# Performance work log

Hardware: AMD Instinct MI355X
Metric: run time of the kernel (lower is better)

The kernel has to match this reference:

```python
import jax, jax.numpy as jnp
import numpy as np

B, F, H, C, K = 4096, 1536, 256, 38, 7  # nodes, feat_dim(effnet_b3), hidden, classes, knn k
EPS = 1e-5  # BatchNorm eps


def setup_inputs() -> dict:
    key = jax.random.key(0)
    ks = jax.random.split(key, 20)
    r = lambda i, shape, s=1.0: jax.random.normal(ks[i], shape, jnp.float32) * s
    u = lambda i, shape: jax.random.uniform(ks[i], shape, jnp.float32, 0.5, 1.5)
    inp = {
        "features": r(0, (B, F)),          # CNN backbone output
        "noise": r(1, (B, B)),             # tie-break noise (scaled by 1e-6 inside)
        # BatchNorm1d on CNN features (eval mode: running stats)
        "bnf_g": jnp.ones((F,)), "bnf_b": jnp.zeros((F,)),
        "bnf_m": r(2, (F,), 0.1), "bnf_v": u(3, (F,)),
        # GCNConv weights
        "W1": r(4, (F, H), 0.02), "b1": jnp.zeros((H,)),
        "W2": r(5, (H, H), 0.05), "b2": jnp.zeros((H,)),
        "W3": r(6, (H, H), 0.05), "b3": jnp.zeros((H,)),
        # PyG BatchNorms (eval mode)
        "bn1_g": jnp.ones((H,)), "bn1_b": jnp.zeros((H,)), "bn1_m": r(7, (H,), 0.1), "bn1_v": u(8, (H,)),
        "bn2_g": jnp.ones((H,)), "bn2_b": jnp.zeros((H,)), "bn2_m": r(9, (H,), 0.1), "bn2_v": u(10, (H,)),
        "bn3_g": jnp.ones((H,)), "bn3_b": jnp.zeros((H,)), "bn3_m": r(11, (H,), 0.1), "bn3_v": u(12, (H,)),
        # classifier MLP
        "Wc1": r(13, (H + F, H // 2), 0.02), "bc1": jnp.zeros((H // 2,)),
        "Wc2": r(14, (H // 2, C), 0.05), "bc2": jnp.zeros((C,)),
    }
    return inp


def _bn(x, g, b, m, v):
    return (x - m) * jax.lax.rsqrt(v + EPS) * g + b


def _knn_edges(x, noise):
    # torch.cdist (p=2) + 1e-6 noise + topk smallest; drop self (col 0)
    sq = jnp.sum(x * x, axis=1)
    d2 = jnp.maximum(sq[:, None] + sq[None, :] - 2.0 * (x @ x.T), 0.0)
    d = jnp.sqrt(d2) + noise * 1e-6
    _, idx = jax.lax.top_k(-d, K + 1)          # smallest K+1 distances
    knn = idx[:, 1:]                           # [B, K] neighbors (col 0 = self)
    src = jnp.repeat(jnp.arange(B), K)         # edge i -> j as in edge_list [[i, j]]
    dst = knn.reshape(-1)
    return src, dst


def _gcn(x, src, dst, W, b):
    # GCNConv: add self-loops, symmetric normalization, aggregate at target (dst)
    h = x @ W
    loop = jnp.arange(B)
    s = jnp.concatenate([src, loop])
    t = jnp.concatenate([dst, loop])
    deg = jnp.zeros((B,), x.dtype).at[t].add(1.0)
    dinv = jax.lax.rsqrt(deg)                  # deg >= 1 due to self-loops
    norm = dinv[s] * dinv[t]
    out = jnp.zeros_like(h).at[t].add(norm[:, None] * h[s])
    return out + b


def reference(features, noise, bnf_g, bnf_b, bnf_m, bnf_v,
              W1, b1, W2, b2, W3, b3,
              bn1_g, bn1_b, bn1_m, bn1_v,
              bn2_g, bn2_b, bn2_m, bn2_v,
              bn3_g, bn3_b, bn3_m, bn3_v,
              Wc1, bc1, Wc2, bc2):
    # CNN head: BN (eval) + dropout(identity in eval)
    x = _bn(features, bnf_g, bnf_b, bnf_m, bnf_v)
    src, dst = _knn_edges(jax.lax.stop_gradient(x), noise)
    x_orig = x
    h = jax.nn.relu(_bn(_gcn(x, src, dst, W1, b1), bn1_g, bn1_b, bn1_m, bn1_v))
    h = jax.nn.relu(_bn(_gcn(h, src, dst, W2, b2), bn2_g, bn2_b, bn2_m, bn2_v))
    h = _bn(_gcn(h, src, dst, W3, b3), bn3_g, bn3_b, bn3_m, bn3_v)
    # batch = arange(B) => global_mean_pool is identity per node
    comb = jnp.concatenate([h, x_orig], axis=1)        # [B, H+F]
    hid = jax.nn.relu(comb @ Wc1 + bc1)
    return hid @ Wc2 + bc2                             # [B, num_classes]
```

## Files before the change

kernel.cpp:

```cpp
#include <hip/hip_runtime.h>
#include <hip/hip_bf16.h>
#include <math.h>

#define Bn 4096
#define Fn 1536
#define Hn 256
#define Cn 38
#define Kn 7
#define GBK 64
#define NCAND 12

typedef __attribute__((ext_vector_type(8))) short short8;
typedef __attribute__((ext_vector_type(4))) float f32x4;
typedef unsigned long long u64;
typedef unsigned int u32;
typedef unsigned short u16;

__device__ __forceinline__ void gld16(const void* g, void* l) {
  __builtin_amdgcn_global_load_lds((const __attribute__((address_space(1))) unsigned int*)g,
                                   (__attribute__((address_space(3))) unsigned int*)l, 16, 0, 0);
}

__global__ void k_prep(const float* __restrict__ g, const float* __restrict__ b,
                       const float* __restrict__ m, const float* __restrict__ v,
                       double* __restrict__ A64, double* __restrict__ C64) {
  int f = blockIdx.x * 256 + threadIdx.x;
  if (f < Fn) {
    double rs = 1.0 / sqrt((double)v[f] + 1e-5);
    double a = (double)g[f] * rs;
    A64[f] = a;
    C64[f] = (double)b[f] - (double)m[f] * a;
  }
}

__global__ void k_bnsplit(const float* __restrict__ feat, const double* __restrict__ A64,
                          const double* __restrict__ C64,
                          u16* __restrict__ Ah, u16* __restrict__ Al, double* __restrict__ sq,
                          float* __restrict__ deg) {
  int row = blockIdx.x;
  int f0 = threadIdx.x * 8;
  const float* fr = feat + (size_t)row * Fn + f0;
  float4 a = *reinterpret_cast<const float4*>(fr);
  float4 b = *reinterpret_cast<const float4*>(fr + 4);
  float xs[8] = {a.x, a.y, a.z, a.w, b.x, b.y, b.z, b.w};
  short8 hv, lv;
  double ss = 0.0;
#pragma unroll
  for (int k = 0; k < 8; k++) {
    double xd = fma((double)xs[k], A64[f0 + k], C64[f0 + k]);
    ss = fma(xd, xd, ss);
    float x = (float)xd;
    __hip_bfloat16 h = __float2bfloat16(x);
    float hf = __bfloat162float(h);
    __hip_bfloat16 lo = __float2bfloat16(x - hf);
    hv[k] = (short)*reinterpret_cast<u16*>(&h);
    lv[k] = (short)*reinterpret_cast<u16*>(&lo);
  }
  *reinterpret_cast<short8*>(Ah + (size_t)row * Fn + f0) = hv;
  *reinterpret_cast<short8*>(Al + (size_t)row * Fn + f0) = lv;
#pragma unroll
  for (int o = 32; o; o >>= 1) ss += __shfl_down(ss, o);
  __shared__ double red[3];
  if ((threadIdx.x & 63) == 0) red[threadIdx.x >> 6] = ss;
  __syncthreads();
  if (threadIdx.x == 0) { sq[row] = red[0] + red[1] + red[2]; deg[row] = 1.f; }
}

__global__ void k_wsplit_all(
    const float* __restrict__ W1, const float* __restrict__ W2, const float* __restrict__ W3,
    const float* __restrict__ Wc1, const float* __restrict__ Wc2,
    u16* __restrict__ W1th, u16* __restrict__ W1tl, u16* __restrict__ W2th, u16* __restrict__ W2tl,
    u16* __restrict__ W3th, u16* __restrict__ W3tl, u16* __restrict__ Wc1th, u16* __restrict__ Wc1tl,
    u16* __restrict__ Wc2th, u16* __restrict__ Wc2tl) {
  const float* W; u16 *Th, *Tl; int K, N;
  switch (blockIdx.z) {
    case 0: W = W1;  Th = W1th;  Tl = W1tl;  K = Fn;      N = Hn;  break;
    case 1: W = W2;  Th = W2th;  Tl = W2tl;  K = Hn;      N = Hn;  break;
    case 2: W = W3;  Th = W3th;  Tl = W3tl;  K = Hn;      N = Hn;  break;
    case 3: W = Wc1; Th = Wc1th; Tl = Wc1tl; K = Hn + Fn; N = 128; break;
    default: W = Wc2; Th = Wc2th; Tl = Wc2tl; K = 128;    N = Cn;  break;
  }
  int k0 = blockIdx.y * 32, n0 = blockIdx.x * 32;
  if (k0 >= K || n0 >= N) return;
  __shared__ float t[32][33];
  int tx = threadIdx.x & 31, ty = threadIdx.x >> 5;
  for (int p = 0; p < 32; p += 8) {
    int k = k0 + ty + p, n = n0 + tx;
    t[ty + p][tx] = (k < K && n < N) ? W[(size_t)k * N + n] : 0.f;
  }
  __syncthreads();
  for (int p = 0; p < 32; p += 8) {
    int n = n0 + ty + p, k = k0 + tx;
    if (n < N && k < K) {
      float x = t[tx][ty + p];
      __hip_bfloat16 h = __float2bfloat16(x);
      float hf = __bfloat162float(h);
      __hip_bfloat16 lo = __float2bfloat16(x - hf);
      Th[(size_t)n * K + k] = *reinterpret_cast<u16*>(&h);
      Tl[(size_t)n * K + k] = *reinterpret_cast<u16*>(&lo);
    }
  }
}

__global__ __launch_bounds__(256) void k_gram(
    const u16* __restrict__ Ah, const double* __restrict__ sq, u64* __restrict__ part) {
  __shared__ union {
    u16 t[2][4096];
    float c[64 * 65];
  } lds;
  const int tid = threadIdx.x;
  const int w = tid >> 6, l = tid & 63;

  int xcd = blockIdx.x & 7;
  int s = blockIdx.x >> 3;
  int ti, tj;
  if (s < 36) {
    int rem = s, a_ = 0;
#pragma unroll 1
    while (rem >= 8 - a_) { rem -= 8 - a_; a_++; }
    ti = xcd * 8 + a_;
    tj = xcd * 8 + a_ + rem;
  } else {
    int sp = s - 36;
    int q = sp >> 6, r = sp & 63;
    int op, l64;
    if (q < 3) { op = xcd * 3 + q; l64 = r; }
    else       { op = 24 + (xcd >> 1); l64 = ((xcd & 1) << 5) | r; }
    int rem = op, g = 0;
#pragma unroll 1
    while (rem >= 7 - g) { rem -= 7 - g; g++; }
    int gi = g, gj = g + 1 + rem;
    ti = gi * 8 + (l64 >> 3);
    tj = gj * 8 + (l64 & 7);
  }
  const int rA0 = ti * 64, rB0 = tj * 64;
  const int isDiag = (ti == tj);

  f32x4 acc[2][2];
  const f32x4 fz = {0.f, 0.f, 0.f, 0.f};
#pragma unroll
  for (int i = 0; i < 2; i++)
#pragma unroll
    for (int j = 0; j < 2; j++) acc[i][j] = fz;

  const u16* mats[2] = { Ah + (size_t)rA0 * Fn, Ah + (size_t)rB0 * Fn };

  auto stage = [&](int k0) {
#pragma unroll
    for (int q = 0; q < 4; q++) {
      int idx = w * 4 + q;
      int mm = idx >> 3, kh = (idx >> 2) & 1, sg = idx & 3;
      int row = sg * 16 + (l >> 2);
      int colel = ((l & 3) * 8) ^ (((l >> 3) & 3) * 8);
      gld16(mats[mm] + (size_t)row * Fn + k0 + kh * 32 + colel,
            (char*)&lds.t[mm][0] + kh * 4096 + sg * 1024);
    }
  };

  const int cB = ((l >> 4) * 16) ^ (((l >> 1) & 3) * 16);
  const int fr16 = l & 15;

  stage(0);
  const int NT = Fn / GBK;
  for (int kt = 0; kt < NT; kt++) {
    __syncthreads();
#pragma unroll
    for (int kh = 0; kh < 2; kh++) {
      short8 fa[2], fb[2];
#pragma unroll
      for (int i = 0; i < 2; i++) {
        int ar = (w >> 1) * 32 + i * 16 + fr16;
        fa[i] = *reinterpret_cast<const short8*>((const char*)&lds.t[0][0] + kh * 4096 + ar * 64 + cB);
        int br = (w & 1) * 32 + i * 16 + fr16;
        fb[i] = *reinterpret_cast<const short8*>((const char*)&lds.t[1][0] + kh * 4096 + br * 64 + cB);
      }
#pragma unroll
      for (int i = 0; i < 2; i++)
#pragma unroll
        for (int j = 0; j < 2; j++)
          acc[i][j] = __builtin_amdgcn_mfma_f32_16x16x32_bf16(fa[i], fb[j], acc[i][j], 0, 0, 0);
    }
    __syncthreads();
    if (kt + 1 < NT) stage((kt + 1) * GBK);
  }

  const int fr = l & 15, fq = l >> 4;
#pragma unroll
  for (int i = 0; i < 2; i++) {
    int r0 = (w >> 1) * 32 + i * 16 + fq * 4;
#pragma unroll
    for (int j = 0; j < 2; j++) {
      int c0 = (w & 1) * 32 + j * 16 + fr;
#pragma unroll
      for (int gg = 0; gg < 4; gg++)
        lds.c[(r0 + gg) * 65 + c0] = acc[i][j][gg];
    }
  }
  __syncthreads();

  u64 top[8];
#pragma unroll
  for (int k = 0; k < 8; k++) top[k] = ~0ull;
  if (tid < 64) {
    int grow = rA0 + tid;
    float sqr = (float)sq[grow];
#pragma unroll 1
    for (int c = 0; c < 64; c++) {
      int gc = rB0 + c;
      if (gc == grow) continue;
      float gv = lds.c[tid * 65 + c];
      float d2 = fmaxf(sqr + (float)sq[gc] - 2.f * gv, 0.f);
      u64 key = ((u64)__float_as_uint(d2) << 32) | (u32)gc;
      if (key < top[7]) {
        top[7] = key;
#pragma unroll
        for (int k = 7; k > 0; k--)
          if (top[k] < top[k - 1]) { u64 tmp = top[k]; top[k] = top[k - 1]; top[k - 1] = tmp; }
      }
    }
    u64* dst = part + ((size_t)grow * 64 + tj) * 8;
#pragma unroll
    for (int k = 0; k < 8; k++) dst[k] = top[k];
  } else if (tid < 128 && !isDiag) {
    int cl = tid - 64;
    int gcol = rB0 + cl;
    float sqc = (float)sq[gcol];
#pragma unroll 1
    for (int s2 = 0; s2 < 64; s2++) {
      float gv = lds.c[s2 * 65 + cl];
      int gr = rA0 + s2;
      float d2 = fmaxf(sqc + (float)sq[gr] - 2.f * gv, 0.f);
      u64 key = ((u64)__float_as_uint(d2) << 32) | (u32)gr;
      if (key < top[7]) {
        top[7] = key;
#pragma unroll
        for (int k = 7; k > 0; k--)
          if (top[k] < top[k - 1]) { u64 tmp = top[k]; top[k] = top[k - 1]; top[k - 1] = tmp; }
      }
    }
    u64* dst = part + ((size_t)gcol * 64 + ti) * 8;
#pragma unroll
    for (int k = 0; k < 8; k++) dst[k] = top[k];
  }
}

__global__ __launch_bounds__(256) void k_candmerge(const u64* __restrict__ part,
                                                   int* __restrict__ cand) {
  int row = blockIdx.x * 4 + (threadIdx.x >> 6);
  int l = threadIdx.x & 63;
  const u64* p = part + (size_t)row * 512 + (size_t)l * 8;
  u64 e[8];
#pragma unroll
  for (int k = 0; k < 8; k++) e[k] = p[k];
#pragma unroll 1
  for (int rnd = 0; rnd < NCAND; rnd++) {
    u64 m = e[0];
#pragma unroll
    for (int k = 1; k < 8; k++) m = e[k] < m ? e[k] : m;
#pragma unroll
    for (int off = 32; off; off >>= 1) {
      u64 o = __shfl_xor(m, off);
      m = o < m ? o : m;
    }
    if (l == 0) cand[row * NCAND + rnd] = (int)(u32)m;
#pragma unroll
    for (int k = 0; k < 8; k++)
      if (e[k] == m) e[k] = ~0ull;
  }
}

__global__ __launch_bounds__(256) void k_rerank(
    const float* __restrict__ feat, const double* __restrict__ A64,
    const double* __restrict__ C64, const double* __restrict__ sq,
    const float* __restrict__ noise, const int* __restrict__ cand,
    int* __restrict__ knn, float* __restrict__ deg) {
  int row = blockIdx.x;
  int w = threadIdx.x >> 6, l = threadIdx.x & 63;
  double xr[Fn / 64];
  const float* fr = feat + (size_t)row * Fn;
#pragma unroll
  for (int i = 0; i < Fn / 64; i++) {
    int e = l + 64 * i;
    xr[i] = fma((double)fr[e], A64[e], C64[e]);
  }
  __shared__ double dots[NCAND];
  for (int m = w; m < NCAND; m += 4) {
    int c = cand[row * NCAND + m];
    const float* fc = feat + (size_t)c * Fn;
    double s = 0.0;
#pragma unroll
    for (int i = 0; i < Fn / 64; i++) {
      int e = l + 64 * i;
      double xj = fma((double)fc[e], A64[e], C64[e]);
      s = fma(xr[i], xj, s);
    }
#pragma unroll
    for (int off = 32; off; off >>= 1) s += __shfl_xor(s, off);
    if (l == 0) dots[m] = s;
  }
  __syncthreads();
  if (threadIdx.x == 0) {
    double sr = sq[row];
    double bd[Kn]; int bi7[Kn];
#pragma unroll
    for (int k = 0; k < Kn; k++) { bd[k] = 1e300; bi7[k] = 0; }
#pragma unroll 1
    for (int m = 0; m < NCAND; m++) {
      int c = cand[row * NCAND + m];
      double d2 = sr + sq[c] - 2.0 * dots[m];
      d2 = d2 > 0.0 ? d2 : 0.0;
      double d = sqrt(d2) + (double)noise[(size_t)row * Bn + c] * 1e-6;
      if (d < bd[Kn - 1]) {
        bd[Kn - 1] = d; bi7[Kn - 1] = c;
#pragma unroll
        for (int k = Kn - 1; k > 0; k--)
          if (bd[k] < bd[k - 1]) {
            double td = bd[k]; bd[k] = bd[k - 1]; bd[k - 1] = td;
            int ti = bi7[k]; bi7[k] = bi7[k - 1]; bi7[k - 1] = ti;
          }
      }
    }
#pragma unroll
    for (int k = 0; k < Kn; k++) {
      knn[row * Kn + k] = bi7[k];
      atomicAdd(&deg[bi7[k]], 1.f);
    }
  }
}

__global__ void k_dinv(const float* __restrict__ deg, float* __restrict__ dinv) {
  int i = blockIdx.x * 256 + threadIdx.x;
  if (i < Bn) dinv[i] = rsqrtf(deg[i]);
}

__global__ void k_aggsc(const float* __restrict__ h, const int* __restrict__ knn,
                        const float* __restrict__ dinv, float* __restrict__ out) {
  int s = blockIdx.x, f = threadIdx.x;
  float hv = h[(size_t)s * Hn + f] * dinv[s];
#pragma unroll
  for (int k = 0; k < Kn; k++) {
    int t = knn[s * Kn + k];
    atomicAdd(&out[(size_t)t * Hn + f], dinv[t] * hv);
  }
}

__global__ void k_bnact_split(const float* __restrict__ x, const float* __restrict__ g,
                              const float* __restrict__ b, const float* __restrict__ m,
                              const float* __restrict__ v, int relu,
                              u16* __restrict__ oh, u16* __restrict__ ol) {
  size_t i8 = ((size_t)blockIdx.x * 256 + threadIdx.x) * 8;
  int c0 = (int)(i8 & (Hn - 1));
  float4 a = *reinterpret_cast<const float4*>(x + i8);
  float4 bb = *reinterpret_cast<const float4*>(x + i8 + 4);
  float xs[8] = {a.x, a.y, a.z, a.w, bb.x, bb.y, bb.z, bb.w};
  short8 hv, lv;
#pragma unroll
  for (int k = 0; k < 8; k++) {
    int c = c0 + k;
    float val = (xs[k] - m[c]) * rsqrtf(v[c] + 1e-5f) * g[c] + b[c];
    if (relu) val = fmaxf(val, 0.f);
    __hip_bfloat16 h = __float2bfloat16(val);
    float hf = __bfloat162float(h);
    __hip_bfloat16 lo = __float2bfloat16(val - hf);
    hv[k] = (short)*reinterpret_cast<u16*>(&h);
    lv[k] = (short)*reinterpret_cast<u16*>(&lo);
  }
  *reinterpret_cast<short8*>(oh + i8) = hv;
  *reinterpret_cast<short8*>(ol + i8) = lv;
}

__global__ __launch_bounds__(256) void k_mgemm(
    const u16* __restrict__ Ah1, const u16* __restrict__ Al1, int lda1,
    const u16* __restrict__ Ah2, const u16* __restrict__ Al2, int lda2, int Ksplit,
    const u16* __restrict__ Wth, const u16* __restrict__ Wtl,
    const float* __restrict__ bias, float* __restrict__ C, int N, int K, int ep,
    float* __restrict__ C2, const float* __restrict__ dinvp,
    u16* __restrict__ OH, u16* __restrict__ OL) {
  __shared__ u16 tA[2][2][4096];
  __shared__ u16 tB[2][2][4096];
  const int tid = threadIdx.x;
  const int w = tid >> 6, l = tid & 63;
  const int m0 = blockIdx.y * 64, n0 = blockIdx.x * 64;
  const int fr = l & 15, fq = l >> 4;

  f32x4 acc[2][2];
  const f32x4 fz = {0.f, 0.f, 0.f, 0.f};
#pragma unroll
  for (int i = 0; i < 2; i++)
#pragma unroll
    for (int j = 0; j < 2; j++) acc[i][j] = fz;

  auto stage = [&](int buf, int k0) {
#pragma unroll
    for (int q = 0; q < 2; q++) {
      int s = w * 2 + q;
      int kg = k0 + s * 8;
      const u16* ah; const u16* al; int ld; int kk = kg;
      if (kg < Ksplit) { ah = Ah1; al = Al1; ld = lda1; }
      else             { ah = Ah2; al = Al2; ld = lda2; kk = kg - Ksplit; }
      gld16(ah + (size_t)(m0 + l) * ld + kk, (char*)&tA[buf][0][0] + s * 1024);
      gld16(al + (size_t)(m0 + l) * ld + kk, (char*)&tA[buf][1][0] + s * 1024);
      gld16(Wth + (size_t)(n0 + l) * K + kg, (char*)&tB[buf][0][0] + s * 1024);
      gld16(Wtl + (size_t)(n0 + l) * K + kg, (char*)&tB[buf][1][0] + s * 1024);
    }
  };

  stage(0, 0);
  const int NT = K / GBK;
  int cur = 0;
  for (int kt = 0; kt < NT; kt++) {
    __syncthreads();
    if (kt + 1 < NT) stage(cur ^ 1, (kt + 1) * GBK);
#pragma unroll
    for (int kh = 0; kh < 2; kh++) {
      const int kb = (kh * 4 + fq) * 1024;
      short8 fa[2][2], fb[2][2];
#pragma unroll
      for (int i = 0; i < 2; i++) {
        int ar = (w >> 1) * 32 + i * 16 + fr;
        fa[0][i] = *reinterpret_cast<const short8*>((const char*)&tA[cur][0][0] + kb + ar * 16);
        fa[1][i] = *reinterpret_cast<const short8*>((const char*)&tA[cur][1][0] + kb + ar * 16);
        int br = (w & 1) * 32 + i * 16 + fr;
        fb[0][i] = *reinterpret_cast<const short8*>((const char*)&tB[cur][0][0] + kb + br * 16);
        fb[1][i] = *reinterpret_cast<const short8*>((const char*)&tB[cur][1][0] + kb + br * 16);
      }
#pragma unroll
      for (int i = 0; i < 2; i++)
#pragma unroll
        for (int j = 0; j < 2; j++) {
          acc[i][j] = __builtin_amdgcn_mfma_f32_16x16x32_bf16(fa[1][i], fb[0][j], acc[i][j], 0, 0, 0);
          acc[i][j] = __builtin_amdgcn_mfma_f32_16x16x32_bf16(fa[0][i], fb[1][j], acc[i][j], 0, 0, 0);
          acc[i][j] = __builtin_amdgcn_mfma_f32_16x16x32_bf16(fa[0][i], fb[0][j], acc[i][j], 0, 0, 0);
        }
    }
    cur ^= 1;
  }

#pragma unroll
  for (int i = 0; i < 2; i++) {
    int rg0 = m0 + (w >> 1) * 32 + i * 16 + fq * 4;
#pragma unroll
    for (int j = 0; j < 2; j++) {
      int cg = n0 + (w & 1) * 32 + j * 16 + fr;
      if (cg >= N) continue;
      float bv = (ep >= 1) ? bias[cg] : 0.f;
#pragma unroll
      for (int g = 0; g < 4; g++) {
        float raw = acc[i][j][g];
        size_t idx = (size_t)(rg0 + g) * N + cg;
        if (ep == 3) {
          float di = dinvp[rg0 + g];
          C[idx] = raw;
          C2[idx] = di * di * raw + bv;
        } else if (ep == 4) {
          float val = fmaxf(raw + bv, 0.f);
          __hip_bfloat16 h = __float2bfloat16(val);
          float hf = __bfloat162float(h);
          __hip_bfloat16 lo = __float2bfloat16(val - hf);
          OH[idx] = *reinterpret_cast<u16*>(&h);
          OL[idx] = *reinterpret_cast<u16*>(&lo);
        } else {
          float val = raw + bv;
          if (ep == 2) val = fmaxf(val, 0.f);
          C[idx] = val;
        }
      }
    }
  }
}

extern "C" void kernel_launch(void* const* d_in, const int* in_sizes, int n_in,
                              void* d_out, int out_size, void* d_ws, size_t ws_size,
                              hipStream_t stream) {
  const float* feat  = (const float*)d_in[0];
  const float* noise = (const float*)d_in[1];
  const float* bnf_g = (const float*)d_in[2];
  const float* bnf_b = (const float*)d_in[3];
  const float* bnf_m = (const float*)d_in[4];
  const float* bnf_v = (const float*)d_in[5];
  const float* W1 = (const float*)d_in[6];
  const float* b1 = (const float*)d_in[7];
  const float* W2 = (const float*)d_in[8];
  const float* b2 = (const float*)d_in[9];
  const float* W3 = (const float*)d_in[10];
  const float* b3 = (const float*)d_in[11];
  const float* bn1_g = (const float*)d_in[12];
  const float* bn1_b = (const float*)d_in[13];
  const float* bn1_m = (const float*)d_in[14];
  const float* bn1_v = (const float*)d_in[15];
  const float* bn2_g = (const float*)d_in[16];
  const float* bn2_b = (const float*)d_in[17];
  const float* bn2_m = (const float*)d_in[18];
  const float* bn2_v = (const float*)d_in[19];
  const float* bn3_g = (const float*)d_in[20];
  const float* bn3_b = (const float*)d_in[21];
  const float* bn3_m = (const float*)d_in[22];
  const float* bn3_v = (const float*)d_in[23];
  const float* Wc1 = (const float*)d_in[24];
  const float* bc1 = (const float*)d_in[25];
  const float* Wc2 = (const float*)d_in[26];
  const float* bc2 = (const float*)d_in[27];
  float* outp = (float*)d_out;

  char* w = (char*)d_ws;
  size_t off = 0;
  auto alloc = [&](size_t n) { void* p = w + off; off = (off + n + 255) & ~(size_t)255; return p; };
  u16*    Ahb  = (u16*)   alloc((size_t)Bn * Fn * 2);
  u16*    Alb  = (u16*)   alloc((size_t)Bn * Fn * 2);
  double* A64  = (double*)alloc(Fn * 8);
  double* C64  = (double*)alloc(Fn * 8);
  double* sq   = (double*)alloc(Bn * 8);
  u64*    part = (u64*)   alloc((size_t)Bn * 64 * 8 * 8);
  int*    cand = (int*)   alloc((size_t)Bn * NCAND * 4);
  int*    knn  = (int*)   alloc((size_t)Bn * Kn * 4);
  float*  deg  = (float*) alloc(Bn * 4);
  float*  dinv = (float*) alloc(Bn * 4);
  float*  g1   = (float*) alloc((size_t)Bn * Hn * 4);
  float*  g2   = (float*) alloc((size_t)Bn * Hn * 4);
  u16*    sh   = (u16*)   alloc((size_t)Bn * Hn * 2);
  u16*    sl   = (u16*)   alloc((size_t)Bn * Hn * 2);
  u16*    hidh = (u16*)   alloc((size_t)Bn * 128 * 2);
  u16*    hidl = (u16*)   alloc((size_t)Bn * 128 * 2);
  u16*    W1th = (u16*)   alloc((size_t)Fn * Hn * 2);
  u16*    W1tl = (u16*)   alloc((size_t)Fn * Hn * 2);
  u16*    W2th = (u16*)   alloc((size_t)Hn * Hn * 2);
  u16*    W2tl = (u16*)   alloc((size_t)Hn * Hn * 2);
  u16*    W3th = (u16*)   alloc((size_t)Hn * Hn * 2);
  u16*    W3tl = (u16*)   alloc((size_t)Hn * Hn * 2);
  u16*    Wc1th= (u16*)   alloc((size_t)(Hn + Fn) * 128 * 2);
  u16*    Wc1tl= (u16*)   alloc((size_t)(Hn + Fn) * 128 * 2);
  u16*    Wc2th= (u16*)   alloc((size_t)64 * 128 * 2);
  u16*    Wc2tl= (u16*)   alloc((size_t)64 * 128 * 2);
  (void)ws_size; (void)in_sizes; (void)n_in; (void)out_size;

  k_prep<<<(Fn + 255) / 256, 256, 0, stream>>>(bnf_g, bnf_b, bnf_m, bnf_v, A64, C64);
  k_bnsplit<<<Bn, Fn / 8, 0, stream>>>(feat, A64, C64, Ahb, Alb, sq, deg);
  k_wsplit_all<<<dim3(8, 56, 5), 256, 0, stream>>>(W1, W2, W3, Wc1, Wc2,
                                                   W1th, W1tl, W2th, W2tl, W3th, W3tl,
                                                   Wc1th, Wc1tl, Wc2th, Wc2tl);

  k_gram<<<2080, 256, 0, stream>>>(Ahb, sq, part);
  k_candmerge<<<Bn / 4, 256, 0, stream>>>(part, cand);
  k_rerank<<<Bn, 256, 0, stream>>>(feat, A64, C64, sq, noise, cand, knn, deg);
  k_dinv<<<(Bn + 255) / 256, 256, 0, stream>>>(deg, dinv);

  dim3 gm(Hn / 64, Bn / 64);
  k_mgemm<<<gm, 256, 0, stream>>>(Ahb, Alb, Fn, Ahb, Alb, Fn, Fn, W1th, W1tl, b1, g1, Hn, Fn, 3,
                                  g2, dinv, nullptr, nullptr);
  k_aggsc<<<Bn, Hn, 0, stream>>>(g1, knn, dinv, g2);
  k_bnact_split<<<(Bn * Hn) / (256 * 8), 256, 0, stream>>>(g2, bn1_g, bn1_b, bn1_m, bn1_v, 1, sh, sl);
  k_mgemm<<<gm, 256, 0, stream>>>(sh, sl, Hn, sh, sl, Hn, Hn, W2th, W2tl, b2, g1, Hn, Hn, 3,
                                  g2, dinv, nullptr, nullptr);
  k_aggsc<<<Bn, Hn, 0, stream>>>(g1, knn, dinv, g2);
  k_bnact_split<<<(Bn * Hn) / (256 * 8), 256, 0, stream>>>(g2, bn2_g, bn2_b, bn2_m, bn2_v, 1, sh, sl);
  k_mgemm<<<gm, 256, 0, stream>>>(sh, sl, Hn, sh, sl, Hn, Hn, W3th, W3tl, b3, g1, Hn, Hn, 3,
                                  g2, dinv, nullptr, nullptr);
  k_aggsc<<<Bn, Hn, 0, stream>>>(g1, knn, dinv, g2);
  k_bnact_split<<<(Bn * Hn) / (256 * 8), 256, 0, stream>>>(g2, bn3_g, bn3_b, bn3_m, bn3_v, 0, sh, sl);
  k_mgemm<<<dim3(128 / 64, Bn / 64), 256, 0, stream>>>(sh, sl, Hn, Ahb, Alb, Fn, Hn,
                                                       Wc1th, Wc1tl, bc1, nullptr, 128, Hn + Fn, 4,
                                                       nullptr, nullptr, hidh, hidl);
  k_mgemm<<<dim3(1, Bn / 64), 256, 0, stream>>>(hidh, hidl, 128, hidh, hidl, 128, 128,
                                                Wc2th, Wc2tl, bc2, outp, Cn, 128, 1,
                                                nullptr, nullptr, nullptr, nullptr);
}
```

Measured before the change: 528.9 us.

## Double gram K-tile depth, drop LDS swizzle, vectorize rerank loads

The gram kernel's K tile grows from 64 to 128, so LDS per operand doubles and the number of barrier-separated iterations halves. The XOR swizzle on the LDS layout is removed, which may bring back bank conflicts on fragment reads. The rerank kernel now reads features as float4 with a contiguous per-lane layout, giving fewer, wider loads. The GEMM kernel hardcodes its tile step of 64 so it stays as before.

```diff
diff --git a/kernel.cpp b/kernel.cpp
--- a/kernel.cpp
+++ b/kernel.cpp
@@ -7,7 +7,7 @@
 #define Hn 256
 #define Cn 38
 #define Kn 7
-#define GBK 64
+#define GBK 128
 #define NCAND 12
 
 typedef __attribute__((ext_vector_type(8))) short short8;
@@ -105,7 +105,7 @@
 __global__ __launch_bounds__(256) void k_gram(
     const u16* __restrict__ Ah, const double* __restrict__ sq, u64* __restrict__ part) {
   __shared__ union {
-    u16 t[2][4096];
+    u16 t[2][8192];
     float c[64 * 65];
   } lds;
   const int tid = threadIdx.x;
@@ -147,17 +147,17 @@
 
   auto stage = [&](int k0) {
 #pragma unroll
-    for (int q = 0; q < 4; q++) {
-      int idx = w * 4 + q;
-      int mm = idx >> 3, kh = (idx >> 2) & 1, sg = idx & 3;
+    for (int q = 0; q < 8; q++) {
+      int idx = w * 8 + q;
+      int mm = idx >> 4, kh = (idx >> 2) & 3, sg = idx & 3;
       int row = sg * 16 + (l >> 2);
-      int colel = ((l & 3) * 8) ^ (((l >> 3) & 3) * 8);
+      int colel = (l & 3) * 8;
       gld16(mats[mm] + (size_t)row * Fn + k0 + kh * 32 + colel,
             (char*)&lds.t[mm][0] + kh * 4096 + sg * 1024);
     }
   };
 
-  const int cB = ((l >> 4) * 16) ^ (((l >> 1) & 3) * 16);
+  const int cB = (l >> 4) * 16;
   const int fr16 = l & 15;
 
   stage(0);
@@ -165,7 +165,7 @@
   for (int kt = 0; kt < NT; kt++) {
     __syncthreads();
 #pragma unroll
-    for (int kh = 0; kh < 2; kh++) {
+    for (int kh = 0; kh < 4; kh++) {
       short8 fa[2], fb[2];
 #pragma unroll
       for (int i = 0; i < 2; i++) {
@@ -276,12 +276,16 @@
     int* __restrict__ knn, float* __restrict__ deg) {
   int row = blockIdx.x;
   int w = threadIdx.x >> 6, l = threadIdx.x & 63;
-  double xr[Fn / 64];
+  double xr[24];
   const float* fr = feat + (size_t)row * Fn;
 #pragma unroll
-  for (int i = 0; i < Fn / 64; i++) {
-    int e = l + 64 * i;
-    xr[i] = fma((double)fr[e], A64[e], C64[e]);
+  for (int i = 0; i < 6; i++) {
+    int e = (l + 64 * i) * 4;
+    float4 xv = *reinterpret_cast<const float4*>(fr + e);
+    xr[i * 4 + 0] = fma((double)xv.x, A64[e + 0], C64[e + 0]);
+    xr[i * 4 + 1] = fma((double)xv.y, A64[e + 1], C64[e + 1]);
+    xr[i * 4 + 2] = fma((double)xv.z, A64[e + 2], C64[e + 2]);
+    xr[i * 4 + 3] = fma((double)xv.w, A64[e + 3], C64[e + 3]);
   }
   __shared__ double dots[NCAND];
   for (int m = w; m < NCAND; m += 4) {
@@ -289,10 +293,13 @@
     const float* fc = feat + (size_t)c * Fn;
     double s = 0.0;
 #pragma unroll
-    for (int i = 0; i < Fn / 64; i++) {
-      int e = l + 64 * i;
-      double xj = fma((double)fc[e], A64[e], C64[e]);
-      s = fma(xr[i], xj, s);
+    for (int i = 0; i < 6; i++) {
+      int e = (l + 64 * i) * 4;
+      float4 yv = *reinterpret_cast<const float4*>(fc + e);
+      s = fma(xr[i * 4 + 0], fma((double)yv.x, A64[e + 0], C64[e + 0]), s);
+      s = fma(xr[i * 4 + 1], fma((double)yv.y, A64[e + 1], C64[e + 1]), s);
+      s = fma(xr[i * 4 + 2], fma((double)yv.z, A64[e + 2], C64[e + 2]), s);
+      s = fma(xr[i * 4 + 3], fma((double)yv.w, A64[e + 3], C64[e + 3]), s);
     }
 #pragma unroll
     for (int off = 32; off; off >>= 1) s += __shfl_xor(s, off);
@@ -406,11 +413,11 @@
   };
 
   stage(0, 0);
-  const int NT = K / GBK;
+  const int NT = K / 64;
   int cur = 0;
   for (int kt = 0; kt < NT; kt++) {
     __syncthreads();
-    if (kt + 1 < NT) stage(cur ^ 1, (kt + 1) * GBK);
+    if (kt + 1 < NT) stage(cur ^ 1, (kt + 1) * 64);
 #pragma unroll
     for (int kh = 0; kh < 2; kh++) {
       const int kb = (kh * 4 + fq) * 1024;
```

Result: slower. 605.3 us (+14.5%).
